# Kernel tuning notes

Hardware: AMD Instinct MI355X
Metric: run time of the kernel (lower is better)

The kernel has to match this reference:

```python
import jax, jax.numpy as jnp
import numpy as np

TURBO_BLOCK_SIZE = 64
TURBO_MSE_BITS = 5
QMAX = 2 ** (TURBO_MSE_BITS - 1) - 1  # 15 for symmetric int5
# MSE scale search grid: shrink factors applied to the max-abs scale
SHRINKS = np.linspace(0.4, 1.0, 16)


def mse_quant_dequant(w):
    """Block-wise (block=64, along input dim) symmetric int5 quantize-dequantize.
    Per block, searches a grid of shrunken max-abs scales and keeps the one
    minimizing reconstruction MSE."""
    O, I = w.shape
    wb = w.reshape(O, I // TURBO_BLOCK_SIZE, TURBO_BLOCK_SIZE)
    amax = jnp.max(jnp.abs(wb), axis=-1, keepdims=True)
    base = jnp.maximum(amax, 1e-8) / QMAX
    best_err = jnp.full(amax.shape, jnp.inf, dtype=w.dtype)
    best_scale = base
    for s in SHRINKS:  # fixed small grid, not a data-dim loop
        scale = base * jnp.asarray(s, dtype=w.dtype)
        deq = jnp.clip(jnp.round(wb / scale), -QMAX, QMAX) * scale
        err = jnp.sum((deq - wb) ** 2, axis=-1, keepdims=True)
        upd = err < best_err
        best_err = jnp.where(upd, err, best_err)
        best_scale = jnp.where(upd, scale, best_scale)
    deq = jnp.clip(jnp.round(wb / best_scale), -QMAX, QMAX) * best_scale
    return deq.reshape(O, I)


def turbo_linear(x, w):
    # Straight-through estimator: forward uses quantized weights,
    # gradient flows to w as identity.
    wq = w + jax.lax.stop_gradient(mse_quant_dequant(w) - w)
    return x @ wq.T


def setup_inputs() -> dict:
    key = jax.random.key(0)
    k1, k2, k3 = jax.random.split(key, 3)
    dim, mlp_mult = 2048, 4
    hidden = mlp_mult * dim
    x = jax.random.normal(k1, (4, 2048, dim), dtype=jnp.float32)
    w_fc = jax.random.normal(k2, (hidden, dim), dtype=jnp.float32) * 0.02
    w_proj = jax.random.normal(k3, (dim, hidden), dtype=jnp.float32) * 0.02
    return {"x": x, "w_fc": w_fc, "w_proj": w_proj}


def reference(x, w_fc, w_proj):
    h = jnp.maximum(turbo_linear(x, w_fc), 0.0)  # relu
    return turbo_linear(h * h, w_proj)           # relu-square then proj
```

## Files before the change

kernel.cpp:

```cpp
#include <hip/hip_runtime.h>
#include <hip/hip_bf16.h>

typedef __attribute__((ext_vector_type(8))) __bf16 bf16x8;
typedef __attribute__((ext_vector_type(4))) float f32x4;

__device__ __forceinline__ void gload_lds16(const void* g, void* lds) {
    __builtin_amdgcn_global_load_lds(
        (const __attribute__((address_space(1))) void*)g,
        (__attribute__((address_space(3))) void*)lds, 16, 0, 0);
}

__global__ __launch_bounds__(256) void quant_bf16_kernel(
    const float* __restrict__ w, __hip_bfloat16* __restrict__ wq, int nblk)
{
#pragma clang fp contract(off)
    int b = blockIdx.x * 256 + threadIdx.x;
    if (b >= nblk) return;
    const float4* src = (const float4*)(w + (size_t)b * 64);
    float v[64];
#pragma unroll
    for (int i = 0; i < 16; ++i) {
        float4 t = src[i];
        v[i*4+0] = t.x; v[i*4+1] = t.y; v[i*4+2] = t.z; v[i*4+3] = t.w;
    }
    float amax = 0.0f;
#pragma unroll
    for (int i = 0; i < 64; ++i) amax = fmaxf(amax, fabsf(v[i]));
    float base = fmaxf(amax, 1e-8f) / 15.0f;

    float best_err = __builtin_inff();
    float best_scale = base, best_rs = 0.0f;
    for (int k = 0; k < 16; ++k) {
        double sd = (k == 15) ? 1.0 : ((double)k * (0.6 / 15.0) + 0.4);
        float scale = base * (float)sd;
        float rs = 1.0f / scale;
        float err = 0.0f;
#pragma unroll
        for (int i = 0; i < 64; ++i) {
            float q = rintf(v[i] * rs);
            q = fminf(fmaxf(q, -15.0f), 15.0f);
            float d = q * scale - v[i];
            err = err + d * d;
        }
        if (err < best_err) { best_err = err; best_scale = scale; best_rs = rs; }
    }
    __hip_bfloat16* dst = wq + (size_t)b * 64;
#pragma unroll
    for (int i = 0; i < 64; ++i) {
        float q = rintf(v[i] * best_rs);
        q = fminf(fmaxf(q, -15.0f), 15.0f);
        dst[i] = __float2bfloat16(q * best_scale);
    }
}

__global__ __launch_bounds__(256) void f32_to_bf16_kernel(
    const float* __restrict__ in, __hip_bfloat16* __restrict__ out, int n8)
{
    int i = blockIdx.x * 256 + threadIdx.x;
    if (i >= n8) return;
    const float4* p = (const float4*)(in + (size_t)i * 8);
    float4 a = p[0], b = p[1];
    alignas(16) __hip_bfloat16 r[8];
    r[0] = __float2bfloat16(a.x); r[1] = __float2bfloat16(a.y);
    r[2] = __float2bfloat16(a.z); r[3] = __float2bfloat16(a.w);
    r[4] = __float2bfloat16(b.x); r[5] = __float2bfloat16(b.y);
    r[6] = __float2bfloat16(b.z); r[7] = __float2bfloat16(b.w);
    *(uint4*)(out + (size_t)i * 8) = *(const uint4*)r;
}

#define LDA2(d, base, s) { \
    d[0] = *(const bf16x8*)(smem + (base) + aB + (s)*2048u + cb0); \
    d[1] = *(const bf16x8*)(smem + (base) + aB + (s)*2048u + cb1); }

#define LDB8(base) { \
    bf[0][0] = *(const bf16x8*)(smem + (base) + bB + 0u    + cb0); \
    bf[0][1] = *(const bf16x8*)(smem + (base) + bB + 0u    + cb1); \
    bf[1][0] = *(const bf16x8*)(smem + (base) + bB + 2048u + cb0); \
    bf[1][1] = *(const bf16x8*)(smem + (base) + bB + 2048u + cb1); \
    bf[2][0] = *(const bf16x8*)(smem + (base) + bB + 4096u + cb0); \
    bf[2][1] = *(const bf16x8*)(smem + (base) + bB + 4096u + cb1); \
    bf[3][0] = *(const bf16x8*)(smem + (base) + bB + 6144u + cb0); \
    bf[3][1] = *(const bf16x8*)(smem + (base) + bB + 6144u + cb1); }

#define MF8(q, a2) { \
    acc[q][0] = __builtin_amdgcn_mfma_f32_16x16x32_bf16(a2[0], bf[0][0], acc[q][0],0,0,0); \
    acc[q][0] = __builtin_amdgcn_mfma_f32_16x16x32_bf16(a2[1], bf[0][1], acc[q][0],0,0,0); \
    acc[q][1] = __builtin_amdgcn_mfma_f32_16x16x32_bf16(a2[0], bf[1][0], acc[q][1],0,0,0); \
    acc[q][1] = __builtin_amdgcn_mfma_f32_16x16x32_bf16(a2[1], bf[1][1], acc[q][1],0,0,0); \
    acc[q][2] = __builtin_amdgcn_mfma_f32_16x16x32_bf16(a2[0], bf[2][0], acc[q][2],0,0,0); \
    acc[q][2] = __builtin_amdgcn_mfma_f32_16x16x32_bf16(a2[1], bf[2][1], acc[q][2],0,0,0); \
    acc[q][3] = __builtin_amdgcn_mfma_f32_16x16x32_bf16(a2[0], bf[3][0], acc[q][3],0,0,0); \
    acc[q][3] = __builtin_amdgcn_mfma_f32_16x16x32_bf16(a2[1], bf[3][1], acc[q][3],0,0,0); }

#define STAGE(base, eoff, ldsOff) \
    gload_lds16((base) + (size_t)((eoff) + voff), smem + (ldsOff) + wOff)

#define BARRIER() { __builtin_amdgcn_sched_barrier(0); \
    __builtin_amdgcn_s_barrier(); __builtin_amdgcn_sched_barrier(0); }

template <int EPI>
__global__ __launch_bounds__(512, 1) void gemm256_kernel(
    const __hip_bfloat16* __restrict__ A,
    const __hip_bfloat16* __restrict__ B,
    void* __restrict__ Cout, int M, int N, int K)
{
    extern __shared__ char smem[];

    const int t    = threadIdx.x;
    const int lane = t & 63;
    const int w    = t >> 6;
    const int wr   = w >> 2;
    const int wc   = w & 3;
    const int lo   = lane & 15;
    const int hi   = lane >> 4;
    const uint wOff = (uint)w * 1024u;

    const int cpx = gridDim.x >> 3;
    int bid = blockIdx.x;
    bid = (bid & 7) * cpx + (bid >> 3);
    const int nN = N >> 8;
    const int bm = bid / nN;
    const int bn = bid % nN;
    const int rowBase = bm << 8;
    const int colBase = bn << 8;

    const __hip_bfloat16* uA = A + (size_t)rowBase * (size_t)K;
    const __hip_bfloat16* uB = B + (size_t)colBase * (size_t)K;
    uint o0 = (uint)t * 16u;
    uint p0 = o0 ^ (((o0 >> 7) & 7u) << 4);
    const uint voff = (p0 >> 7) * (uint)K + ((p0 & 127u) >> 1);
    const uint K64 = (uint)K * 64u;

    const uint sw  = (uint)(lo & 7) << 4;
    const uint aB  = (uint)wr * 16384u + (uint)lo * 128u;
    const uint bB  = 32768u + (uint)(wc >> 1) * 16384u
                   + ((uint)(wc & 1) * 64u + (uint)lo) * 128u;
    const uint cb0 = ((uint)hi * 16u) ^ sw;
    const uint cb1 = (64u + (uint)hi * 16u) ^ sw;

    f32x4 acc[8][4] = {};
    bf16x8 aC0[2], aC1[2], bf[4][2];

    STAGE(uA, 0u,        0u);       STAGE(uA, K64,        8192u);
    STAGE(uA, 2u*K64,    16384u);   STAGE(uA, 3u*K64,     24576u);
    STAGE(uB, 0u,        32768u);   STAGE(uB, K64,        40960u);
    STAGE(uB, 2u*K64,    49152u);   STAGE(uB, 3u*K64,     57344u);
    STAGE(uB, 64u,           98304u);  STAGE(uB, K64 + 64u,     106496u);
    STAGE(uB, 2u*K64 + 64u, 114688u);  STAGE(uB, 3u*K64 + 64u,  122880u);
    asm volatile("s_waitcnt vmcnt(4)" ::: "memory");
    BARRIER();
    LDA2(aC0, 0u, 0u); LDA2(aC1, 0u, 1u); LDB8(0u);

    const int NI = K >> 7;
    for (int P = 0; P < NI; ++P) {
        const bool pf = (P + 1 < NI);
        const uint kN1 = ((uint)(2 * P + 1)) << 6;
        const uint kN2 = kN1 + 64u;
        const uint kN3 = kN1 + 128u;

        STAGE(uA, kN1,       65536u);  STAGE(uA, kN1 + K64, 73728u);
        __builtin_amdgcn_s_setprio(1);
        MF8(0, aC0); LDA2(aC0, 0u, 2u);
        MF8(1, aC1); LDA2(aC1, 0u, 3u);
        __builtin_amdgcn_s_setprio(0);
        BARRIER();

        STAGE(uA, kN1 + 2u*K64, 81920u);  STAGE(uA, kN1 + 3u*K64, 90112u);
        __builtin_amdgcn_s_setprio(1);
        MF8(2, aC0); LDA2(aC0, 0u, 4u);
        MF8(3, aC1); LDA2(aC1, 0u, 5u);
        __builtin_amdgcn_s_setprio(0);
        BARRIER();

        if (pf) { STAGE(uB, kN2, 32768u); STAGE(uB, kN2 + K64, 40960u); }
        __builtin_amdgcn_s_setprio(1);
        MF8(4, aC0); LDA2(aC0, 0u, 6u);
        MF8(5, aC1); LDA2(aC1, 0u, 7u);
        __builtin_amdgcn_s_setprio(0);
        if (pf) asm volatile("s_waitcnt vmcnt(2)" ::: "memory");
        else    asm volatile("s_waitcnt vmcnt(0)" ::: "memory");
        BARRIER();

        if (pf) { STAGE(uB, kN2 + 2u*K64, 49152u); STAGE(uB, kN2 + 3u*K64, 57344u); }
        __builtin_amdgcn_s_setprio(1);
        MF8(6, aC0); LDA2(aC0, 65536u, 0u);
        MF8(7, aC1); LDA2(aC1, 65536u, 1u);
        __builtin_amdgcn_s_setprio(0);
        LDB8(65536u);
        BARRIER();

        if (pf) { STAGE(uA, kN2, 0u); STAGE(uA, kN2 + K64, 8192u); }
        __builtin_amdgcn_s_setprio(1);
        MF8(0, aC0); LDA2(aC0, 65536u, 2u);
        MF8(1, aC1); LDA2(aC1, 65536u, 3u);
        __builtin_amdgcn_s_setprio(0);
        BARRIER();

        if (pf) { STAGE(uA, kN2 + 2u*K64, 16384u); STAGE(uA, kN2 + 3u*K64, 24576u); }
        __builtin_amdgcn_s_setprio(1);
        MF8(2, aC0); LDA2(aC0, 65536u, 4u);
        MF8(3, aC1); LDA2(aC1, 65536u, 5u);
        __builtin_amdgcn_s_setprio(0);
        BARRIER();

        if (pf) { STAGE(uB, kN3, 98304u); STAGE(uB, kN3 + K64, 106496u); }
        __builtin_amdgcn_s_setprio(1);
        MF8(4, aC0); LDA2(aC0, 65536u, 6u);
        MF8(5, aC1); LDA2(aC1, 65536u, 7u);
        __builtin_amdgcn_s_setprio(0);
        if (pf) asm volatile("s_waitcnt vmcnt(2)" ::: "memory");
        BARRIER();

        if (pf) { STAGE(uB, kN3 + 2u*K64, 114688u); STAGE(uB, kN3 + 3u*K64, 122880u); }
        __builtin_amdgcn_s_setprio(1);
        MF8(6, aC0); if (pf) LDA2(aC0, 0u, 0u);
        MF8(7, aC1); if (pf) LDA2(aC1, 0u, 1u);
        __builtin_amdgcn_s_setprio(0);
        if (pf) LDB8(0u);
        BARRIER();
    }

    if (EPI == 0) {
        __hip_bfloat16* Cb = (__hip_bfloat16*)Cout;
#pragma unroll
        for (int i = 0; i < 8; ++i)
#pragma unroll
            for (int j = 0; j < 4; ++j)
#pragma unroll
                for (int r = 0; r < 4; ++r) {
                    size_t row = rowBase + wr*128 + i*16 + hi*4 + r;
                    size_t col = colBase + wc*64 + j*16 + lo;
                    float v = fmaxf(acc[i][j][r], 0.0f);
                    Cb[row * N + col] = __float2bfloat16(v * v);
                }
    } else {
        float* Cf = (float*)Cout;
#pragma unroll
        for (int i = 0; i < 8; ++i)
#pragma unroll
            for (int j = 0; j < 4; ++j)
#pragma unroll
                for (int r = 0; r < 4; ++r) {
                    size_t row = rowBase + wr*128 + i*16 + hi*4 + r;
                    size_t col = colBase + wc*64 + j*16 + lo;
                    Cf[row * N + col] = acc[i][j][r];
                }
    }
}

extern "C" void kernel_launch(void* const* d_in, const int* in_sizes, int n_in,
                              void* d_out, int out_size, void* d_ws, size_t ws_size,
                              hipStream_t stream) {
    const float* x      = (const float*)d_in[0];
    const float* w_fc   = (const float*)d_in[1];
    const float* w_proj = (const float*)d_in[2];
    float* out = (float*)d_out;

    const int DIM = 2048, HID = 8192, M = 8192;

    char* ws = (char*)d_ws;
    __hip_bfloat16* Xb  = (__hip_bfloat16*)ws;
    __hip_bfloat16* Wfc = (__hip_bfloat16*)(ws + (size_t)M * DIM * 2);
    __hip_bfloat16* Wpj = (__hip_bfloat16*)(ws + (size_t)(M * DIM + (size_t)HID * DIM) * 2);
    __hip_bfloat16* H2  = (__hip_bfloat16*)(ws + (size_t)(M * DIM + 2 * (size_t)HID * DIM) * 2);

    (void)hipFuncSetAttribute((const void*)gemm256_kernel<0>,
                              hipFuncAttributeMaxDynamicSharedMemorySize, 131072);
    (void)hipFuncSetAttribute((const void*)gemm256_kernel<1>,
                              hipFuncAttributeMaxDynamicSharedMemorySize, 131072);

    int nblk = HID * DIM / 64;
    quant_bf16_kernel<<<nblk / 256, 256, 0, stream>>>(w_fc, Wfc, nblk);
    quant_bf16_kernel<<<nblk / 256, 256, 0, stream>>>(w_proj, Wpj, nblk);

    int n8 = M * DIM / 8;
    f32_to_bf16_kernel<<<n8 / 256, 256, 0, stream>>>(x, Xb, n8);

    gemm256_kernel<0><<<(M/256)*(HID/256), 512, 131072, stream>>>(
        Xb, Wfc, (void*)H2, M, HID, DIM);

    gemm256_kernel<1><<<(M/256)*(DIM/256), 512, 131072, stream>>>(
        H2, Wpj, (void*)out, M, DIM, HID);
}
```

Baseline: 590.1 us.

## Replace fine-grained interleaved GEMM pipeline with simple double-buffered K loop

Replaces the hand-scheduled 8-phase main loop, which staggered partial A/B tile loads across phases with multiple barriers, with a plain double buffer. Each iteration prefetches the whole next 64-wide K tile into the other LDS half, runs all MFMAs on the current half, then waits on vmcnt(0) and barriers once. This removes most barriers and simplifies the schedule. In exchange, global loads only overlap with one tile of compute and there is a full drain every iteration, so memory latency may be less hidden.

```diff
diff --git a/kernel.cpp b/kernel.cpp
--- a/kernel.cpp
+++ b/kernel.cpp
@@ -141,82 +141,56 @@
     f32x4 acc[8][4] = {};
     bf16x8 aC0[2], aC1[2], bf[4][2];
 
-    STAGE(uA, 0u,        0u);       STAGE(uA, K64,        8192u);
-    STAGE(uA, 2u*K64,    16384u);   STAGE(uA, 3u*K64,     24576u);
-    STAGE(uB, 0u,        32768u);   STAGE(uB, K64,        40960u);
-    STAGE(uB, 2u*K64,    49152u);   STAGE(uB, 3u*K64,     57344u);
-    STAGE(uB, 64u,           98304u);  STAGE(uB, K64 + 64u,     106496u);
-    STAGE(uB, 2u*K64 + 64u, 114688u);  STAGE(uB, 3u*K64 + 64u,  122880u);
-    asm volatile("s_waitcnt vmcnt(4)" ::: "memory");
+    STAGE(uA, 0u,     0u);      STAGE(uA, K64,    8192u);
+    STAGE(uA, 2u*K64, 16384u);  STAGE(uA, 3u*K64, 24576u);
+    STAGE(uB, 0u,     32768u);  STAGE(uB, K64,    40960u);
+    STAGE(uB, 2u*K64, 49152u);  STAGE(uB, 3u*K64, 57344u);
+    asm volatile("s_waitcnt vmcnt(0)" ::: "memory");
     BARRIER();
-    LDA2(aC0, 0u, 0u); LDA2(aC1, 0u, 1u); LDB8(0u);
-
-    const int NI = K >> 7;
-    for (int P = 0; P < NI; ++P) {
-        const bool pf = (P + 1 < NI);
-        const uint kN1 = ((uint)(2 * P + 1)) << 6;
-        const uint kN2 = kN1 + 64u;
-        const uint kN3 = kN1 + 128u;
-
-        STAGE(uA, kN1,       65536u);  STAGE(uA, kN1 + K64, 73728u);
-        __builtin_amdgcn_s_setprio(1);
-        MF8(0, aC0); LDA2(aC0, 0u, 2u);
-        MF8(1, aC1); LDA2(aC1, 0u, 3u);
-        __builtin_amdgcn_s_setprio(0);
-        BARRIER();
-
-        STAGE(uA, kN1 + 2u*K64, 81920u);  STAGE(uA, kN1 + 3u*K64, 90112u);
-        __builtin_amdgcn_s_setprio(1);
-        MF8(2, aC0); LDA2(aC0, 0u, 4u);
-        MF8(3, aC1); LDA2(aC1, 0u, 5u);
-        __builtin_amdgcn_s_setprio(0);
-        BARRIER();
-
-        if (pf) { STAGE(uB, kN2, 32768u); STAGE(uB, kN2 + K64, 40960u); }
-        __builtin_amdgcn_s_setprio(1);
-        MF8(4, aC0); LDA2(aC0, 0u, 6u);
-        MF8(5, aC1); LDA2(aC1, 0u, 7u);
-        __builtin_amdgcn_s_setprio(0);
-        if (pf) asm volatile("s_waitcnt vmcnt(2)" ::: "memory");
-        else    asm volatile("s_waitcnt vmcnt(0)" ::: "memory");
-        BARRIER();
-
-        if (pf) { STAGE(uB, kN2 + 2u*K64, 49152u); STAGE(uB, kN2 + 3u*K64, 57344u); }
-        __builtin_amdgcn_s_setprio(1);
-        MF8(6, aC0); LDA2(aC0, 65536u, 0u);
-        MF8(7, aC1); LDA2(aC1, 65536u, 1u);
-        __builtin_amdgcn_s_setprio(0);
-        LDB8(65536u);
-        BARRIER();
-
-        if (pf) { STAGE(uA, kN2, 0u); STAGE(uA, kN2 + K64, 8192u); }
-        __builtin_amdgcn_s_setprio(1);
-        MF8(0, aC0); LDA2(aC0, 65536u, 2u);
-        MF8(1, aC1); LDA2(aC1, 65536u, 3u);
-        __builtin_amdgcn_s_setprio(0);
-        BARRIER();
-
-        if (pf) { STAGE(uA, kN2 + 2u*K64, 16384u); STAGE(uA, kN2 + 3u*K64, 24576u); }
-        __builtin_amdgcn_s_setprio(1);
-        MF8(2, aC0); LDA2(aC0, 65536u, 4u);
-        MF8(3, aC1); LDA2(aC1, 65536u, 5u);
-        __builtin_amdgcn_s_setprio(0);
-        BARRIER();
-
-        if (pf) { STAGE(uB, kN3, 98304u); STAGE(uB, kN3 + K64, 106496u); }
-        __builtin_amdgcn_s_setprio(1);
-        MF8(4, aC0); LDA2(aC0, 65536u, 6u);
-        MF8(5, aC1); LDA2(aC1, 65536u, 7u);
-        __builtin_amdgcn_s_setprio(0);
-        if (pf) asm volatile("s_waitcnt vmcnt(2)" ::: "memory");
-        BARRIER();
-
-        if (pf) { STAGE(uB, kN3 + 2u*K64, 114688u); STAGE(uB, kN3 + 3u*K64, 122880u); }
-        __builtin_amdgcn_s_setprio(1);
-        MF8(6, aC0); if (pf) LDA2(aC0, 0u, 0u);
-        MF8(7, aC1); if (pf) LDA2(aC1, 0u, 1u);
-        __builtin_amdgcn_s_setprio(0);
-        if (pf) LDB8(0u);
+
+    const int NT = K >> 6;
+    for (int tt = 0; tt < NT; ++tt) {
+        const uint bufOff = (uint)(tt & 1) * 65536u;
+        const uint nxtOff = bufOff ^ 65536u;
+        const bool pf = (tt + 1 < NT);
+        const uint kN = ((uint)(tt + 1)) << 6;
+
+        if (pf) {
+            STAGE(uA, kN,          nxtOff + 0u);
+            STAGE(uA, kN + K64,    nxtOff + 8192u);
+            STAGE(uA, kN + 2u*K64, nxtOff + 16384u);
+            STAGE(uA, kN + 3u*K64, nxtOff + 24576u);
+            STAGE(uB, kN,          nxtOff + 32768u);
+            STAGE(uB, kN + K64,    nxtOff + 40960u);
+            STAGE(uB, kN + 2u*K64, nxtOff + 49152u);
+            STAGE(uB, kN + 3u*K64, nxtOff + 57344u);
+        }
+        __builtin_amdgcn_sched_barrier(0);
+
+        LDB8(bufOff);
+        LDA2(aC0, bufOff, 0u); LDA2(aC1, bufOff, 1u);
+
+        __builtin_amdgcn_s_setprio(1);
+        MF8(0, aC0); LDA2(aC0, bufOff, 2u);
+        MF8(1, aC1); LDA2(aC1, bufOff, 3u);
+        __builtin_amdgcn_s_setprio(0);
+
+        __builtin_amdgcn_s_setprio(1);
+        MF8(2, aC0); LDA2(aC0, bufOff, 4u);
+        MF8(3, aC1); LDA2(aC1, bufOff, 5u);
+        __builtin_amdgcn_s_setprio(0);
+
+        __builtin_amdgcn_s_setprio(1);
+        MF8(4, aC0); LDA2(aC0, bufOff, 6u);
+        MF8(5, aC1); LDA2(aC1, bufOff, 7u);
+        __builtin_amdgcn_s_setprio(0);
+
+        __builtin_amdgcn_s_setprio(1);
+        MF8(6, aC0);
+        MF8(7, aC1);
+        __builtin_amdgcn_s_setprio(0);
+
+        if (pf) asm volatile("s_waitcnt vmcnt(0)" ::: "memory");
         BARRIER();
     }
 
```

New measurement: 606.6 us. +2.8%, slower.
